# Kernel tuning notes

Hardware: AMD Instinct MI355X
Metric: run time of the kernel (lower is better)

Reference implementation:

```python
import jax, jax.numpy as jnp
import numpy as np

D_MODEL = 768; HEADS = 12; DEPTH = 12; PATCH = 16; IMG = 224; NCLS = 1000
N_PATCH = (IMG // PATCH) ** 2  # 196
N_TOK = N_PATCH + 1            # 197 (cls token)
REGION = 16                    # tokens per routing region
TOPK = 4                       # regions gathered per query region


def layernorm(x, g, b, eps=1e-5):
    mu = jnp.mean(x, -1, keepdims=True)
    var = jnp.mean((x - mu) ** 2, -1, keepdims=True)
    return (x - mu) * jax.lax.rsqrt(var + eps) * g + b


def biformer_attn(h, qkv_w, qkv_b, proj_w, proj_b):
    # Bi-Level Routing Attention: region-mean routing + top-k region gather.
    B, N, C = h.shape
    dh = C // HEADS
    qkv = h @ qkv_w + qkv_b                      # [B,N,3C]
    pad = (-N) % REGION
    qkv = jnp.pad(qkv, ((0, 0), (0, pad), (0, 0)))
    Np = N + pad; R = Np // REGION
    q, k, v = jnp.split(qkv, 3, axis=-1)
    qr = q.reshape(B, R, REGION, C)
    kr = k.reshape(B, R, REGION, C)
    vr = v.reshape(B, R, REGION, C)
    # coarse region-level affinity from region means
    q_reg = qr.mean(2); k_reg = kr.mean(2)       # [B,R,C]
    aff = jnp.einsum('brc,bsc->brs', q_reg, k_reg)
    _, idx = jax.lax.top_k(aff, TOPK)            # [B,R,TOPK] int32
    gather = jax.vmap(lambda t, i: t[i])         # gather regions per batch elem
    kg = gather(kr, idx).reshape(B, R, TOPK * REGION, C)
    vg = gather(vr, idx).reshape(B, R, TOPK * REGION, C)
    # fine-grained attention within each region over gathered keys
    qh = qr.reshape(B, R, REGION, HEADS, dh)
    kh = kg.reshape(B, R, TOPK * REGION, HEADS, dh)
    vh = vg.reshape(B, R, TOPK * REGION, HEADS, dh)
    att = jnp.einsum('brmhd,brnhd->bhrmn', qh, kh) * (dh ** -0.5)
    att = jax.nn.softmax(att, axis=-1)
    out = jnp.einsum('bhrmn,brnhd->brmhd', att, vh).reshape(B, Np, C)[:, :N]
    return out @ proj_w + proj_b


def _forward(x, conv_w, conv_b, cls_token, pos_embed,
             ln1_g, ln1_b, qkv_w, qkv_b, proj_w, proj_b,
             ln2_g, ln2_b, fc1_w, fc1_b, fc2_w, fc2_b, head_w, head_b):
    B = x.shape[0]
    p = jax.lax.conv_general_dilated(
        x, conv_w, (PATCH, PATCH), 'VALID',
        dimension_numbers=('NCHW', 'OIHW', 'NCHW')) + conv_b[None, :, None, None]
    t = p.reshape(B, D_MODEL, N_PATCH).transpose(0, 2, 1)   # [B,196,C]
    t = jnp.concatenate([jnp.broadcast_to(cls_token, (B, 1, D_MODEL)), t], axis=1)
    t = t + pos_embed                                        # [B,197,C]

    def block(xc, pp):
        g1, b1, qw, qb, pw, pb, g2, b2, f1w, f1b, f2w, f2b = pp
        h = layernorm(xc, g1, b1)
        h = biformer_attn(h, qw, qb, pw, pb)
        h = layernorm(h, g2, b2)
        h = jax.nn.gelu(h @ f1w + f1b, approximate=False) @ f2w + f2b
        return xc + h, None   # single residual around LN-Attn-LN-MLP (as in source)

    blk = (ln1_g, ln1_b, qkv_w, qkv_b, proj_w, proj_b,
           ln2_g, ln2_b, fc1_w, fc1_b, fc2_w, fc2_b)
    t, _ = jax.lax.scan(block, t, blk)
    return t[:, 0] @ head_w + head_b


def setup_inputs() -> dict:
    key = jax.random.key(0)
    ks = jax.random.split(key, 10)
    B = 16; s = 0.02
    f32 = jnp.float32
    return {
        'x': jax.random.normal(ks[0], (B, 3, IMG, IMG), f32),
        'conv_w': jax.random.normal(ks[1], (D_MODEL, 3, PATCH, PATCH), f32) * s,
        'conv_b': jnp.zeros((D_MODEL,), f32),
        'cls_token': jax.random.normal(ks[2], (1, 1, D_MODEL), f32) * s,
        'pos_embed': jax.random.normal(ks[3], (1, N_TOK, D_MODEL), f32) * s,
        'ln1_g': jnp.ones((DEPTH, D_MODEL), f32),
        'ln1_b': jnp.zeros((DEPTH, D_MODEL), f32),
        'qkv_w': jax.random.normal(ks[4], (DEPTH, D_MODEL, 3 * D_MODEL), f32) * s,
        'qkv_b': jnp.zeros((DEPTH, 3 * D_MODEL), f32),
        'proj_w': jax.random.normal(ks[5], (DEPTH, D_MODEL, D_MODEL), f32) * s,
        'proj_b': jnp.zeros((DEPTH, D_MODEL), f32),
        'ln2_g': jnp.ones((DEPTH, D_MODEL), f32),
        'ln2_b': jnp.zeros((DEPTH, D_MODEL), f32),
        'fc1_w': jax.random.normal(ks[6], (DEPTH, D_MODEL, 4 * D_MODEL), f32) * s,
        'fc1_b': jnp.zeros((DEPTH, 4 * D_MODEL), f32),
        'fc2_w': jax.random.normal(ks[7], (DEPTH, 4 * D_MODEL, D_MODEL), f32) * s,
        'fc2_b': jnp.zeros((DEPTH, D_MODEL), f32),
        'head_w': jax.random.normal(ks[8], (D_MODEL, NCLS), f32) * s,
        'head_b': jnp.zeros((NCLS,), f32),
    }


def reference(x, conv_w, conv_b, cls_token, pos_embed,
              ln1_g, ln1_b, qkv_w, qkv_b, proj_w, proj_b,
              ln2_g, ln2_b, fc1_w, fc1_b, fc2_w, fc2_b, head_w, head_b):
    return _forward(x, conv_w, conv_b, cls_token, pos_embed,
                    ln1_g, ln1_b, qkv_w, qkv_b, proj_w, proj_b,
                    ln2_g, ln2_b, fc1_w, fc1_b, fc2_w, fc2_b, head_w, head_b)
```

## Files before the change

### kernel.cpp

```cpp
#include <hip/hip_runtime.h>
#include <hip/hip_bf16.h>
#include <math.h>


typedef __bf16 bf16_t;
typedef __bf16 bf16x8 __attribute__((ext_vector_type(8)));
typedef __bf16 bf16x4 __attribute__((ext_vector_type(4)));
typedef __bf16 bf16x2v __attribute__((ext_vector_type(2)));
typedef float floatx4 __attribute__((ext_vector_type(4)));

static __device__ __forceinline__ float b2f(bf16_t x) { return (float)x; }
static __device__ __forceinline__ bf16_t f2b(float x) { return (bf16_t)x; }

#define AS1q __attribute__((address_space(1)))
#define AS3q __attribute__((address_space(3)))
static __device__ __forceinline__ void gll16(const bf16_t* g, bf16_t* l) {
    __builtin_amdgcn_global_load_lds((const AS1q void*)g, (AS3q void*)l, 16, 0, 0);
}

__global__ void transpose_split(const float* __restrict__ in, bf16_t* __restrict__ oh,
                                bf16_t* __restrict__ ol, int R, int C) {
    __shared__ float tile[32][33];
    int c0 = blockIdx.x * 32, r0 = blockIdx.y * 32;
    int tx = threadIdx.x, ty = threadIdx.y;
#pragma unroll
    for (int i = 0; i < 4; i++) {
        int r = r0 + ty + i * 8;
        float v = 0.f;
        if (r < R && (c0 + tx) < C) v = in[(size_t)r * C + c0 + tx];
        tile[ty + i * 8][tx] = v;
    }
    __syncthreads();
#pragma unroll
    for (int i = 0; i < 4; i++) {
        int c = c0 + ty + i * 8;
        if (c < C && (r0 + tx) < R) {
            float v = tile[tx][ty + i * 8];
            bf16_t h = f2b(v);
            oh[(size_t)c * R + r0 + tx] = h;
            ol[(size_t)c * R + r0 + tx] = f2b(v - b2f(h));
        }
    }
}

__global__ void split_kernel(const float* __restrict__ in, bf16_t* __restrict__ oh,
                             bf16_t* __restrict__ ol, int n) {
    int id = blockIdx.x * 256 + threadIdx.x;
    if (id < n) {
        float v = in[id];
        bf16_t h = f2b(v);
        oh[id] = h;
        ol[id] = f2b(v - b2f(h));
    }
}

__global__ void im2col_split(const float* __restrict__ x, bf16_t* __restrict__ oh,
                             bf16_t* __restrict__ ol) {
    int id = blockIdx.x * 256 + threadIdx.x;
    if (id >= 3136 * 768) return;
    int col = id % 768, row = id / 768;
    int b = row / 196, p = row % 196;
    int py = p / 14, px = p % 14;
    int c = col >> 8, rem = col & 255, ky = rem >> 4, kx = rem & 15;
    float v = x[(((size_t)(b * 3 + c)) * 224 + (py * 16 + ky)) * 224 + (px * 16 + kx)];
    bf16_t h = f2b(v);
    oh[id] = h;
    ol[id] = f2b(v - b2f(h));
}

__global__ void clspos_kernel(const float* __restrict__ cls, const float* __restrict__ pos,
                              float* __restrict__ t) {
    int id = blockIdx.x * 256 + threadIdx.x;
    int b = id / 768, c = id % 768;
    t[((size_t)(b * 197)) * 768 + c] = cls[c] + pos[c];
}

__global__ __launch_bounds__(256) void ln_kernel(const float* __restrict__ in,
                                                 const float* __restrict__ g,
                                                 const float* __restrict__ bb,
                                                 bf16_t* __restrict__ oh,
                                                 bf16_t* __restrict__ ol,
                                                 float* __restrict__ outf) {
    int row = blockIdx.x;
    int t = threadIdx.x;
    const float* x = in + (size_t)row * 768;
    float v0 = x[t], v1 = x[t + 256], v2 = x[t + 512];
    float s = v0 + v1 + v2;
#pragma unroll
    for (int off = 32; off > 0; off >>= 1) s += __shfl_down(s, off, 64);
    __shared__ float red[8];
    int lane = t & 63, wave = t >> 6;
    if (lane == 0) red[wave] = s;
    __syncthreads();
    float mu = (red[0] + red[1] + red[2] + red[3]) * (1.f / 768.f);
    float d0 = v0 - mu, d1 = v1 - mu, d2 = v2 - mu;
    float vs = d0 * d0 + d1 * d1 + d2 * d2;
#pragma unroll
    for (int off = 32; off > 0; off >>= 1) vs += __shfl_down(vs, off, 64);
    if (lane == 0) red[4 + wave] = vs;
    __syncthreads();
    float var = (red[4] + red[5] + red[6] + red[7]) * (1.f / 768.f);
    float rstd = 1.0f / sqrtf(var + 1e-5f);
    float y0 = d0 * rstd * g[t] + bb[t];
    float y1 = d1 * rstd * g[t + 256] + bb[t + 256];
    float y2 = d2 * rstd * g[t + 512] + bb[t + 512];
    size_t base = (size_t)row * 768;
    bf16_t h0 = f2b(y0), h1 = f2b(y1), h2 = f2b(y2);
    oh[base + t] = h0; oh[base + t + 256] = h1; oh[base + t + 512] = h2;
    ol[base + t] = f2b(y0 - b2f(h0));
    ol[base + t + 256] = f2b(y1 - b2f(h1));
    ol[base + t + 512] = f2b(y2 - b2f(h2));
    if (outf) {
        outf[base + t] = y0; outf[base + t + 256] = y1; outf[base + t + 512] = y2;
    }
}

__global__ __launch_bounds__(256) void gemm_nts(const bf16_t* __restrict__ Ah,
                                                const bf16_t* __restrict__ Al,
                                                const bf16_t* __restrict__ Bh,
                                                const bf16_t* __restrict__ Bl,
                                                const float* __restrict__ bias,
                                                float* __restrict__ outF,
                                                bf16_t* __restrict__ outHi,
                                                bf16_t* __restrict__ outLo,
                                                int M, int N, int K, int Kc,
                                                size_t pstride, int mode) {
    __shared__ __align__(16) bf16_t Ash[2][128 * 32];
    __shared__ __align__(16) bf16_t Asl[2][128 * 32];
    __shared__ __align__(16) bf16_t Bsh[2][128 * 32];
    __shared__ __align__(16) bf16_t Bsl[2][128 * 32];
    const int t = threadIdx.x;
    const int lane = t & 63, wave = t >> 6;
    const int quad = lane >> 4, l16 = lane & 15;
    const int wm = (wave >> 1) * 64, wn = (wave & 1) * 64;
    const int m0 = blockIdx.y * 128, n0 = blockIdx.x * 128;
    const int kz = blockIdx.z;

    floatx4 acc[4][4];
#pragma unroll
    for (int i = 0; i < 4; i++)
#pragma unroll
        for (int j = 0; j < 4; j++)
#pragma unroll
            for (int p = 0; p < 4; p++) acc[i][j][p] = 0.f;

    const int sr = wave * 16 + (lane >> 2);
    const int sc = (lane & 3) * 8;
    const size_t a0 = (size_t)(m0 + sr) * K + sc;
    const size_t a1 = (size_t)(m0 + 64 + sr) * K + sc;
    const size_t b0 = (size_t)(n0 + sr) * K + sc;
    const size_t b1 = (size_t)(n0 + 64 + sr) * K + sc;
    const int lo0 = wave * 512;
    const int lo1 = 2048 + wave * 512;

    auto stage = [&](int buf, int k) {
        gll16(Ah + a0 + k, &Ash[buf][lo0]);
        gll16(Ah + a1 + k, &Ash[buf][lo1]);
        gll16(Al + a0 + k, &Asl[buf][lo0]);
        gll16(Al + a1 + k, &Asl[buf][lo1]);
        gll16(Bh + b0 + k, &Bsh[buf][lo0]);
        gll16(Bh + b1 + k, &Bsh[buf][lo1]);
        gll16(Bl + b0 + k, &Bsl[buf][lo0]);
        gll16(Bl + b1 + k, &Bsl[buf][lo1]);
    };
    auto compute = [&](int buf) {
        bf16x8 ah[4], al[4], bh[4], bl[4];
#pragma unroll
        for (int i = 0; i < 4; i++) {
            ah[i] = *(const bf16x8*)&Ash[buf][(wm + i * 16 + l16) * 32 + quad * 8];
            al[i] = *(const bf16x8*)&Asl[buf][(wm + i * 16 + l16) * 32 + quad * 8];
        }
#pragma unroll
        for (int j = 0; j < 4; j++) {
            bh[j] = *(const bf16x8*)&Bsh[buf][(wn + j * 16 + l16) * 32 + quad * 8];
            bl[j] = *(const bf16x8*)&Bsl[buf][(wn + j * 16 + l16) * 32 + quad * 8];
        }
#pragma unroll
        for (int i = 0; i < 4; i++)
#pragma unroll
            for (int j = 0; j < 4; j++) {
                acc[i][j] = __builtin_amdgcn_mfma_f32_16x16x32_bf16(ah[i], bh[j], acc[i][j], 0, 0, 0);
                acc[i][j] = __builtin_amdgcn_mfma_f32_16x16x32_bf16(ah[i], bl[j], acc[i][j], 0, 0, 0);
                acc[i][j] = __builtin_amdgcn_mfma_f32_16x16x32_bf16(al[i], bh[j], acc[i][j], 0, 0, 0);
            }
    };

    const int kbeg = kz * Kc, kend = kbeg + Kc;
    stage(0, kbeg);
    __syncthreads();
    int cur = 0;
    for (int k0 = kbeg + 32; k0 < kend; k0 += 32) {
        stage(cur ^ 1, k0);
        compute(cur);
        __syncthreads();
        cur ^= 1;
    }
    compute(cur);

    float* Pp = outF + (size_t)kz * pstride;
#pragma unroll
    for (int i = 0; i < 4; i++) {
#pragma unroll
        for (int p = 0; p < 4; p++) {
            int m = m0 + wm + i * 16 + quad * 4 + p;
            if (m >= M) continue;
#pragma unroll
            for (int j = 0; j < 4; j++) {
                int n = n0 + wn + j * 16 + l16;
                if (n >= N) continue;
                if (mode == 0) {
                    Pp[(size_t)m * N + n] = acc[i][j][p];
                } else if (mode == 1) {
                    outF[(size_t)m * N + n] = acc[i][j][p] + bias[n];
                } else {
                    float v = acc[i][j][p] + bias[n];
                    float gl = 0.5f * v * (1.0f + erff(v * 0.70710678118654752f));
                    bf16_t h = f2b(gl);
                    outHi[(size_t)m * N + n] = h;
                    outLo[(size_t)m * N + n] = f2b(gl - b2f(h));
                }
            }
        }
    }
}

__global__ void reduce_kernel(const float* __restrict__ parts, int nchunks,
                              const float* __restrict__ bias, float* __restrict__ out,
                              const float* __restrict__ pos, int M, int N, int mode) {
    int id = blockIdx.x * 256 + threadIdx.x;
    int total = (M * N) >> 2;
    if (id >= total) return;
    size_t e = (size_t)id * 4;
    int n = (int)(e % N), m = (int)(e / N);
    size_t csz = (size_t)M * N;
    floatx4 s = *(const floatx4*)(parts + e);
    for (int c = 1; c < nchunks; c++) s += *(const floatx4*)(parts + (size_t)c * csz + e);
    s += *(const floatx4*)(bias + n);
    if (mode == 0) {
        *(floatx4*)(out + e) = s;
    } else if (mode == 1) {
        floatx4 o = *(const floatx4*)(out + e);
        *(floatx4*)(out + e) = o + s;
    } else {
        int b = m / 196, p = m % 196;
        floatx4 pv = *(const floatx4*)(pos + (size_t)(1 + p) * N + n);
        *(floatx4*)(out + ((size_t)(b * 197 + 1 + p)) * N + n) = s + pv;
    }
}

__global__ __launch_bounds__(256) void reduce_ln_kernel(const float* __restrict__ parts,
                                                        int nchunks, size_t cstride,
                                                        const float* __restrict__ bias,
                                                        const float* __restrict__ g,
                                                        const float* __restrict__ bb,
                                                        bf16_t* __restrict__ oh,
                                                        bf16_t* __restrict__ ol) {
    int row = blockIdx.x;
    int t = threadIdx.x;
    float y0, y1, y2;
    {
        size_t base = (size_t)row * 768;
        float a0 = bias[t], a1 = bias[t + 256], a2 = bias[t + 512];
        for (int c = 0; c < nchunks; c++) {
            const float* p = parts + (size_t)c * cstride + base;
            a0 += p[t]; a1 += p[t + 256]; a2 += p[t + 512];
        }
        y0 = a0; y1 = a1; y2 = a2;
    }
    float s = y0 + y1 + y2;
#pragma unroll
    for (int off = 32; off > 0; off >>= 1) s += __shfl_down(s, off, 64);
    __shared__ float red[8];
    int lane = t & 63, wave = t >> 6;
    if (lane == 0) red[wave] = s;
    __syncthreads();
    float mu = (red[0] + red[1] + red[2] + red[3]) * (1.f / 768.f);
    float d0 = y0 - mu, d1 = y1 - mu, d2 = y2 - mu;
    float vs = d0 * d0 + d1 * d1 + d2 * d2;
#pragma unroll
    for (int off = 32; off > 0; off >>= 1) vs += __shfl_down(vs, off, 64);
    if (lane == 0) red[4 + wave] = vs;
    __syncthreads();
    float var = (red[4] + red[5] + red[6] + red[7]) * (1.f / 768.f);
    float rstd = 1.0f / sqrtf(var + 1e-5f);
    float z0 = d0 * rstd * g[t] + bb[t];
    float z1 = d1 * rstd * g[t + 256] + bb[t + 256];
    float z2 = d2 * rstd * g[t + 512] + bb[t + 512];
    size_t base = (size_t)row * 768;
    bf16_t h0 = f2b(z0), h1 = f2b(z1), h2 = f2b(z2);
    oh[base + t] = h0; oh[base + t + 256] = h1; oh[base + t + 512] = h2;
    ol[base + t] = f2b(z0 - b2f(h0));
    ol[base + t + 256] = f2b(z1 - b2f(h1));
    ol[base + t + 512] = f2b(z2 - b2f(h2));
}

__global__ void regsum_kernel(const float* __restrict__ h, float* __restrict__ hsum) {
    int bid = blockIdx.x;
    int b = bid / 13, r = bid % 13;
    int t = threadIdx.x;
#pragma unroll
    for (int j = 0; j < 3; j++) {
        int c = t + j * 256;
        float s = 0.f;
        for (int tt = 0; tt < 16; tt++) {
            int tp = r * 16 + tt;
            if (tp < 197) s += h[((size_t)(b * 197 + tp)) * 768 + c];
        }
        hsum[(size_t)bid * 768 + c] = s;
    }
}

__global__ __launch_bounds__(256) void qkreg_gemm(const float* __restrict__ hsum,
                                                  const float* __restrict__ W,
                                                  const float* __restrict__ bias,
                                                  float* __restrict__ qreg,
                                                  float* __restrict__ kreg) {
    __shared__ float A_s[16][33];
    __shared__ float B_s[32][68];
    const int t = threadIdx.x;
    const int m0 = blockIdx.y * 16;
    const int n0 = blockIdx.x * 64;
    const int m = t >> 4;
    const int nn = (t & 15) * 4;
    floatx4 acc;
    acc[0] = acc[1] = acc[2] = acc[3] = 0.f;

    for (int k0 = 0; k0 < 768; k0 += 32) {
        {
            int c = (t & 15) * 2;
            A_s[t >> 4][c]     = hsum[(size_t)(m0 + (t >> 4)) * 768 + k0 + c];
            A_s[t >> 4][c + 1] = hsum[(size_t)(m0 + (t >> 4)) * 768 + k0 + c + 1];
        }
        {
            int kr = t >> 3, cc = (t & 7) * 8;
            const float* src = W + (size_t)(k0 + kr) * 2304 + n0 + cc;
            floatx4 w0 = *(const floatx4*)src;
            floatx4 w1 = *(const floatx4*)(src + 4);
            *(floatx4*)&B_s[kr][cc] = w0;
            *(floatx4*)&B_s[kr][cc + 4] = w1;
        }
        __syncthreads();
#pragma unroll
        for (int kk = 0; kk < 32; kk++) {
            float a = A_s[m][kk];
            floatx4 bv = *(const floatx4*)&B_s[kk][nn];
            acc += a * bv;
        }
        __syncthreads();
    }

    int row = m0 + m;
    int r = row % 13;
    float nr = (r == 12) ? 5.f : 16.f;
#pragma unroll
    for (int j = 0; j < 4; j++) {
        int c = n0 + nn + j;
        float val = (acc[j] + nr * bias[c]) * 0.0625f;
        if (c < 768) qreg[(size_t)row * 768 + c] = val;
        else         kreg[(size_t)row * 768 + (c - 768)] = val;
    }
}

__global__ __launch_bounds__(256) void afftopk_kernel(const float* __restrict__ qreg,
                                                      const float* __restrict__ kreg,
                                                      int* __restrict__ idx) {
    __shared__ float arow[16];
    int br = blockIdx.x;
    int b = br / 13;
    int t = threadIdx.x, lane = t & 63, w = t >> 6;
    const float* qp = qreg + (size_t)br * 768;
    for (int s = w; s < 13; s += 4) {
        const float* kp = kreg + ((size_t)(b * 13 + s)) * 768;
        float a = 0.f;
#pragma unroll
        for (int jj = 0; jj < 3; jj++) {
            floatx4 q4 = *(const floatx4*)&qp[lane * 4 + jj * 256];
            floatx4 k4 = *(const floatx4*)&kp[lane * 4 + jj * 256];
            a += q4[0] * k4[0] + q4[1] * k4[1] + q4[2] * k4[2] + q4[3] * k4[3];
        }
#pragma unroll
        for (int msk = 32; msk >= 1; msk >>= 1) a += __shfl_xor(a, msk, 64);
        if (lane == 0) arow[s] = a;
    }
    __syncthreads();
    if (t == 0) {
        int mask = 0;
#pragma unroll
        for (int k = 0; k < 4; k++) {
            float best = -3.4e38f;
            int bi = 0;
            for (int s = 0; s < 13; s++) {
                if (!((mask >> s) & 1) && arow[s] > best) { best = arow[s]; bi = s; }
            }
            mask |= 1 << bi;
            idx[br * 4 + k] = bi;
        }
    }
}

__global__ __launch_bounds__(256) void attn_kernel(const float* __restrict__ qkv,
                                                   const int* __restrict__ idx,
                                                   bf16_t* __restrict__ oh,
                                                   bf16_t* __restrict__ ol) {
    __shared__ __align__(16) bf16_t Qh[16 * 72], Ql[16 * 72];
    __shared__ __align__(16) bf16_t Kh[64 * 72], Kl[64 * 72];
    __shared__ __align__(16) bf16_t Vth[64 * 68], Vtl[64 * 68];
    __shared__ __align__(16) float P_s[16 * 68];

    int bid = blockIdx.x;
    int head = bid % 12;
    int r = (bid / 12) % 13;
    int b = bid / (12 * 13);
    int t = threadIdx.x;
    const int lane = t & 63, wave = t >> 6;
    const int quad = lane >> 4, l16 = lane & 15;
    const int co = head * 64;
    const size_t rowb = (size_t)(b * 197);

    int regs[4];
#pragma unroll
    for (int j = 0; j < 4; j++) regs[j] = idx[(b * 13 + r) * 4 + j];

    {
        int rh = t >> 5;
        int c2 = (t & 31) * 2;
#pragma unroll
        for (int it = 0; it < 2; it++) {
            int m = rh + it * 8;
            int tp = r * 16 + m;
            float2 v; v.x = 0.f; v.y = 0.f;
            if (tp < 197) v = *(const float2*)&qkv[(rowb + tp) * 2304 + co + c2];
            bf16_t h0 = f2b(v.x), h1 = f2b(v.y);
            bf16x2v hh = {h0, h1};
            bf16x2v ll = {f2b(v.x - b2f(h0)), f2b(v.y - b2f(h1))};
            *(bf16x2v*)&Qh[m * 72 + c2] = hh;
            *(bf16x2v*)&Ql[m * 72 + c2] = ll;
        }
#pragma unroll
        for (int nb = 0; nb < 4; nb++) {
            int reg = regs[nb];
#pragma unroll
            for (int i2 = 0; i2 < 2; i2++) {
                int nn = rh + i2 * 8;
                int tp = reg * 16 + nn;
                int n = nb * 16 + nn;
                float2 v; v.x = 0.f; v.y = 0.f;
                if (tp < 197) v = *(const float2*)&qkv[(rowb + tp) * 2304 + 768 + co + c2];
                bf16_t h0 = f2b(v.x), h1 = f2b(v.y);
                bf16x2v hh = {h0, h1};
                bf16x2v ll = {f2b(v.x - b2f(h0)), f2b(v.y - b2f(h1))};
                *(bf16x2v*)&Kh[n * 72 + c2] = hh;
                *(bf16x2v*)&Kl[n * 72 + c2] = ll;
            }
        }
    }
    {
        int d = lane;
#pragma unroll
        for (int nb = 0; nb < 4; nb++) {
            int reg = regs[nb];
#pragma unroll
            for (int i2 = 0; i2 < 4; i2++) {
                int nn = wave + i2 * 4;
                int tp = reg * 16 + nn;
                int n = nb * 16 + nn;
                float v = (tp < 197) ? qkv[(rowb + tp) * 2304 + 1536 + co + d] : 0.f;
                bf16_t h = f2b(v);
                Vth[d * 68 + n] = h;
                Vtl[d * 68 + n] = f2b(v - b2f(h));
            }
        }
    }
    __syncthreads();

    {
        const int j = wave;
        bf16x8 qfh[2], qfl[2], kfh[2], kfl[2];
#pragma unroll
        for (int ks = 0; ks < 2; ks++) {
            qfh[ks] = *(const bf16x8*)&Qh[l16 * 72 + ks * 32 + quad * 8];
            qfl[ks] = *(const bf16x8*)&Ql[l16 * 72 + ks * 32 + quad * 8];
            kfh[ks] = *(const bf16x8*)&Kh[(j * 16 + l16) * 72 + ks * 32 + quad * 8];
            kfl[ks] = *(const bf16x8*)&Kl[(j * 16 + l16) * 72 + ks * 32 + quad * 8];
        }
        floatx4 s;
        s[0] = s[1] = s[2] = s[3] = 0.f;
#pragma unroll
        for (int ks = 0; ks < 2; ks++) {
            s = __builtin_amdgcn_mfma_f32_16x16x32_bf16(qfh[ks], kfh[ks], s, 0, 0, 0);
            s = __builtin_amdgcn_mfma_f32_16x16x32_bf16(qfh[ks], kfl[ks], s, 0, 0, 0);
            s = __builtin_amdgcn_mfma_f32_16x16x32_bf16(qfl[ks], kfh[ks], s, 0, 0, 0);
        }
#pragma unroll
        for (int p = 0; p < 4; p++)
            P_s[(quad * 4 + p) * 68 + j * 16 + l16] = s[p] * 0.125f;
    }
    __syncthreads();

    {
        int rw = t >> 4, c = t & 15;
        floatx4 v = *(const floatx4*)&P_s[rw * 68 + c * 4];
        float mx = fmaxf(fmaxf(v[0], v[1]), fmaxf(v[2], v[3]));
#pragma unroll
        for (int msk = 8; msk >= 1; msk >>= 1) mx = fmaxf(mx, __shfl_xor(mx, msk, 64));
        floatx4 e;
        e[0] = expf(v[0] - mx); e[1] = expf(v[1] - mx);
        e[2] = expf(v[2] - mx); e[3] = expf(v[3] - mx);
        float sm = e[0] + e[1] + e[2] + e[3];
#pragma unroll
        for (int msk = 8; msk >= 1; msk >>= 1) sm += __shfl_xor(sm, msk, 64);
        float inv = 1.f / sm;
        e[0] *= inv; e[1] *= inv; e[2] *= inv; e[3] *= inv;
        *(floatx4*)&P_s[rw * 68 + c * 4] = e;
    }
    __syncthreads();

    {
        const int j = wave;
        bf16x8 pfh[2], pfl[2], vfh[2], vfl[2];
#pragma unroll
        for (int ks = 0; ks < 2; ks++) {
            floatx4 p0 = *(const floatx4*)&P_s[l16 * 68 + ks * 32 + quad * 8];
            floatx4 p1 = *(const floatx4*)&P_s[l16 * 68 + ks * 32 + quad * 8 + 4];
#pragma unroll
            for (int i = 0; i < 4; i++) {
                float f0 = p0[i], f1 = p1[i];
                bf16_t h0 = f2b(f0), h1 = f2b(f1);
                pfh[ks][i] = h0;      pfh[ks][4 + i] = h1;
                pfl[ks][i] = f2b(f0 - b2f(h0));
                pfl[ks][4 + i] = f2b(f1 - b2f(h1));
            }
            int vrow = (j * 16 + l16) * 68 + ks * 32 + quad * 8;
            bf16x4 a0 = *(const bf16x4*)&Vth[vrow];
            bf16x4 a1 = *(const bf16x4*)&Vth[vrow + 4];
            bf16x4 c0 = *(const bf16x4*)&Vtl[vrow];
            bf16x4 c1 = *(const bf16x4*)&Vtl[vrow + 4];
#pragma unroll
            for (int i = 0; i < 4; i++) {
                vfh[ks][i] = a0[i]; vfh[ks][4 + i] = a1[i];
                vfl[ks][i] = c0[i]; vfl[ks][4 + i] = c1[i];
            }
        }
        floatx4 o;
        o[0] = o[1] = o[2] = o[3] = 0.f;
#pragma unroll
        for (int ks = 0; ks < 2; ks++) {
            o = __builtin_amdgcn_mfma_f32_16x16x32_bf16(pfh[ks], vfh[ks], o, 0, 0, 0);
            o = __builtin_amdgcn_mfma_f32_16x16x32_bf16(pfh[ks], vfl[ks], o, 0, 0, 0);
            o = __builtin_amdgcn_mfma_f32_16x16x32_bf16(pfl[ks], vfh[ks], o, 0, 0, 0);
        }
#pragma unroll
        for (int p = 0; p < 4; p++) {
            int m = quad * 4 + p;
            int tp = r * 16 + m;
            if (tp < 197) {
                size_t oidx = (rowb + tp) * 768 + co + j * 16 + l16;
                float f = o[p];
                bf16_t h = f2b(f);
                oh[oidx] = h;
                ol[oidx] = f2b(f - b2f(h));
            }
        }
    }
}

__global__ void headx_split(const float* __restrict__ t, bf16_t* __restrict__ oh,
                            bf16_t* __restrict__ ol) {
    int id = blockIdx.x * 256 + threadIdx.x;
    if (id >= 16 * 768) return;
    int b = id / 768, c = id % 768;
    float v = t[((size_t)(b * 197)) * 768 + c];
    bf16_t h = f2b(v);
    oh[id] = h;
    ol[id] = f2b(v - b2f(h));
}

extern "C" void kernel_launch(void* const* d_in, const int* in_sizes, int n_in,
                              void* d_out, int out_size, void* d_ws, size_t ws_size,
                              hipStream_t stream) {
    const float* x      = (const float*)d_in[0];
    const float* conv_w = (const float*)d_in[1];
    const float* conv_b = (const float*)d_in[2];
    const float* cls    = (const float*)d_in[3];
    const float* pos    = (const float*)d_in[4];
    const float* ln1g   = (const float*)d_in[5];
    const float* ln1b   = (const float*)d_in[6];
    const float* qkvw   = (const float*)d_in[7];
    const float* qkvb   = (const float*)d_in[8];
    const float* projw  = (const float*)d_in[9];
    const float* projb  = (const float*)d_in[10];
    const float* ln2g   = (const float*)d_in[11];
    const float* ln2b   = (const float*)d_in[12];
    const float* fc1w   = (const float*)d_in[13];
    const float* fc1b   = (const float*)d_in[14];
    const float* fc2w   = (const float*)d_in[15];
    const float* fc2b   = (const float*)d_in[16];
    const float* headw  = (const float*)d_in[17];
    const float* headb  = (const float*)d_in[18];
    float* out = (float*)d_out;

    char* ws = (char*)d_ws;
    size_t off = 0;
    auto alloc = [&](size_t bytes) -> void* {
        void* p = ws + off;
        off += (bytes + 255) & ~(size_t)255;
        return p;
    };
    float*  tbuf   = (float*)alloc((size_t)3152 * 768 * 4);
    float*  h32    = (float*)alloc((size_t)3152 * 768 * 4);
    bf16_t* lnHi   = (bf16_t*)alloc((size_t)3152 * 768 * 2);
    bf16_t* lnLo   = (bf16_t*)alloc((size_t)3152 * 768 * 2);
    bf16_t* atHi   = (bf16_t*)alloc((size_t)3152 * 768 * 2);
    bf16_t* atLo   = (bf16_t*)alloc((size_t)3152 * 768 * 2);
    bf16_t* WhiT   = (bf16_t*)alloc((size_t)3072 * 768 * 2);
    bf16_t* WloT   = (bf16_t*)alloc((size_t)3072 * 768 * 2);
    char*   uni    = (char*)alloc((size_t)3152 * 3072 * 2 * 2);
    float*  qkvF   = (float*)uni;
    bf16_t* geHi   = (bf16_t*)uni;
    bf16_t* geLo   = geHi + (size_t)3152 * 3072;
    bf16_t* imHi   = (bf16_t*)uni;
    bf16_t* imLo   = imHi + (size_t)3136 * 768;
    float*  embPar = (float*)(uni + (size_t)3136 * 768 * 2 * 2);
    float*  hsum   = (float*)alloc((size_t)208 * 768 * 4);
    float*  qreg   = (float*)alloc((size_t)208 * 768 * 4);
    float*  kreg   = (float*)alloc((size_t)208 * 768 * 4);
    int*    idx    = (int*)alloc((size_t)832 * 4);
    bf16_t* hdHi   = (bf16_t*)alloc((size_t)16 * 768 * 2);
    bf16_t* hdLo   = (bf16_t*)alloc((size_t)16 * 768 * 2);
    alloc((size_t)1 << 18);
    if (off > ws_size) return;

    dim3 blk(256);
    dim3 tblk(32, 8);
    const int RED768 = (3152 * 768 / 4) / 256;
    const int REDEMB = (3136 * 768 / 4) / 256;
    const size_t PS = (size_t)3152 * 768;

    im2col_split<<<dim3(9408), blk, 0, stream>>>(x, imHi, imLo);
    split_kernel<<<dim3(2304), blk, 0, stream>>>(conv_w, WhiT, WloT, 768 * 768);
    gemm_nts<<<dim3(6, 25, 3), blk, 0, stream>>>(imHi, imLo, WhiT, WloT, nullptr,
                                                 embPar, nullptr, nullptr,
                                                 3136, 768, 768, 256, (size_t)3136 * 768, 0);
    reduce_kernel<<<dim3(REDEMB), blk, 0, stream>>>(embPar, 3, conv_b, tbuf, pos,
                                                    3136, 768, 2);
    clspos_kernel<<<dim3(48), blk, 0, stream>>>(cls, pos, tbuf);

    for (int l = 0; l < 12; l++) {
        ln_kernel<<<dim3(3152), blk, 0, stream>>>(tbuf, ln1g + l * 768, ln1b + l * 768,
                                                  lnHi, lnLo, h32);

        regsum_kernel<<<dim3(208), blk, 0, stream>>>(h32, hsum);
        qkreg_gemm<<<dim3(24, 13), blk, 0, stream>>>(hsum, qkvw + (size_t)l * 768 * 2304,
                                                     qkvb + l * 2304, qreg, kreg);
        afftopk_kernel<<<dim3(208), blk, 0, stream>>>(qreg, kreg, idx);

        transpose_split<<<dim3(72, 24), tblk, 0, stream>>>(qkvw + (size_t)l * 768 * 2304,
                                                           WhiT, WloT, 768, 2304);
        gemm_nts<<<dim3(18, 25, 1), blk, 0, stream>>>(lnHi, lnLo, WhiT, WloT,
                                                      qkvb + l * 2304, qkvF,
                                                      nullptr, nullptr,
                                                      3152, 2304, 768, 768, 0, 1);

        attn_kernel<<<dim3(16 * 13 * 12), blk, 0, stream>>>(qkvF, idx, atHi, atLo);

        transpose_split<<<dim3(24, 24), tblk, 0, stream>>>(projw + (size_t)l * 768 * 768,
                                                           WhiT, WloT, 768, 768);
        gemm_nts<<<dim3(6, 25, 4), blk, 0, stream>>>(atHi, atLo, WhiT, WloT, nullptr,
                                                     (float*)uni, nullptr, nullptr,
                                                     3152, 768, 768, 192, PS, 0);
        reduce_ln_kernel<<<dim3(3152), blk, 0, stream>>>((float*)uni, 4, PS,
                                                         projb + l * 768,
                                                         ln2g + l * 768, ln2b + l * 768,
                                                         lnHi, lnLo);

        transpose_split<<<dim3(96, 24), tblk, 0, stream>>>(fc1w + (size_t)l * 768 * 3072,
                                                           WhiT, WloT, 768, 3072);
        gemm_nts<<<dim3(24, 25, 1), blk, 0, stream>>>(lnHi, lnLo, WhiT, WloT,
                                                      fc1b + l * 3072, nullptr,
                                                      geHi, geLo, 3152, 3072, 768, 768, 0, 2);

        transpose_split<<<dim3(24, 96), tblk, 0, stream>>>(fc2w + (size_t)l * 3072 * 768,
                                                           WhiT, WloT, 3072, 768);
        gemm_nts<<<dim3(6, 25, 3), blk, 0, stream>>>(geHi, geLo, WhiT, WloT, nullptr,
                                                     h32, nullptr, nullptr,
                                                     3152, 768, 3072, 1024, PS, 0);
        reduce_kernel<<<dim3(RED768), blk, 0, stream>>>(h32, 3, fc2b + l * 768,
                                                        tbuf, nullptr, 3152, 768, 1);
    }

    headx_split<<<dim3(48), blk, 0, stream>>>(tbuf, hdHi, hdLo);
    transpose_split<<<dim3(32, 24), tblk, 0, stream>>>(headw, WhiT, WloT, 768, 1000);
    gemm_nts<<<dim3(8, 1, 3), blk, 0, stream>>>(hdHi, hdLo, WhiT, WloT, nullptr,
                                                hsum, nullptr, nullptr,
                                                16, 1000, 768, 256, (size_t)16 * 1000, 0);
    reduce_kernel<<<dim3(16), blk, 0, stream>>>(hsum, 3, headb, out, nullptr,
                                                16, 1000, 0);
}
```

Baseline: 5.240 ms.

## Batch per-layer weight transposes into one launch and single-buffer GEMM LDS

Replaces the four per-layer transpose_split launches with one transpose_all kernel that converts all of a layer's weights into a larger scratch buffer at distinct offsets, cutting launch count. Separately, the GEMM drops its double-buffered LDS prefetch in favour of a single buffer with syncs before and after each load. That halves LDS use and may allow higher occupancy, but global-load latency is no longer hidden behind MFMA work. The two ideas are unrelated and pull in different directions.

```diff
diff --git a/kernel.cpp b/kernel.cpp
--- a/kernel.cpp
+++ b/kernel.cpp
@@ -17,6 +17,11 @@
 static __device__ __forceinline__ void gll16(const bf16_t* g, bf16_t* l) {
     __builtin_amdgcn_global_load_lds((const AS1q void*)g, (AS3q void*)l, 16, 0, 0);
 }
+
+#define OPRJ 1769472
+#define OFC1 2359296
+#define OFC2 4718592
+#define WTSZ 7077888
 
 __global__ void transpose_split(const float* __restrict__ in, bf16_t* __restrict__ oh,
                                 bf16_t* __restrict__ ol, int R, int C) {
@@ -40,6 +45,34 @@
             oh[(size_t)c * R + r0 + tx] = h;
             ol[(size_t)c * R + r0 + tx] = f2b(v - b2f(h));
         }
+    }
+}
+
+__global__ void transpose_all(const float* __restrict__ qkvw,
+                              const float* __restrict__ projw,
+                              const float* __restrict__ fc1w,
+                              const float* __restrict__ fc2w,
+                              bf16_t* __restrict__ oh, bf16_t* __restrict__ ol) {
+    __shared__ float tile[32][33];
+    int id = blockIdx.x;
+    const float* in; int R, C, ctiles; size_t ooff;
+    if (id < 1728)      { in = qkvw;  R = 768;  C = 2304; ctiles = 72; ooff = 0; }
+    else if (id < 2304) { id -= 1728; in = projw; R = 768;  C = 768;  ctiles = 24; ooff = OPRJ; }
+    else if (id < 4608) { id -= 2304; in = fc1w;  R = 768;  C = 3072; ctiles = 96; ooff = OFC1; }
+    else                { id -= 4608; in = fc2w;  R = 3072; C = 768;  ctiles = 24; ooff = OFC2; }
+    int c0 = (id % ctiles) * 32, r0 = (id / ctiles) * 32;
+    int tx = threadIdx.x, ty = threadIdx.y;
+#pragma unroll
+    for (int i = 0; i < 4; i++)
+        tile[ty + i * 8][tx] = in[(size_t)(r0 + ty + i * 8) * C + c0 + tx];
+    __syncthreads();
+#pragma unroll
+    for (int i = 0; i < 4; i++) {
+        int c = c0 + ty + i * 8;
+        float v = tile[tx][ty + i * 8];
+        bf16_t h = f2b(v);
+        oh[ooff + (size_t)c * R + r0 + tx] = h;
+        ol[ooff + (size_t)c * R + r0 + tx] = f2b(v - b2f(h));
     }
 }
 
@@ -125,10 +158,10 @@
                                                 bf16_t* __restrict__ outLo,
                                                 int M, int N, int K, int Kc,
                                                 size_t pstride, int mode) {
-    __shared__ __align__(16) bf16_t Ash[2][128 * 32];
-    __shared__ __align__(16) bf16_t Asl[2][128 * 32];
-    __shared__ __align__(16) bf16_t Bsh[2][128 * 32];
-    __shared__ __align__(16) bf16_t Bsl[2][128 * 32];
+    __shared__ __align__(16) bf16_t Ash[128 * 32];
+    __shared__ __align__(16) bf16_t Asl[128 * 32];
+    __shared__ __align__(16) bf16_t Bsh[128 * 32];
+    __shared__ __align__(16) bf16_t Bsl[128 * 32];
     const int t = threadIdx.x;
     const int lane = t & 63, wave = t >> 6;
     const int quad = lane >> 4, l16 = lane & 15;
@@ -153,27 +186,28 @@
     const int lo0 = wave * 512;
     const int lo1 = 2048 + wave * 512;
 
-    auto stage = [&](int buf, int k) {
-        gll16(Ah + a0 + k, &Ash[buf][lo0]);
-        gll16(Ah + a1 + k, &Ash[buf][lo1]);
-        gll16(Al + a0 + k, &Asl[buf][lo0]);
-        gll16(Al + a1 + k, &Asl[buf][lo1]);
-        gll16(Bh + b0 + k, &Bsh[buf][lo0]);
-        gll16(Bh + b1 + k, &Bsh[buf][lo1]);
-        gll16(Bl + b0 + k, &Bsl[buf][lo0]);
-        gll16(Bl + b1 + k, &Bsl[buf][lo1]);
-    };
-    auto compute = [&](int buf) {
+    const int kend = kz * Kc + Kc;
+    for (int k0 = kz * Kc; k0 < kend; k0 += 32) {
+        __syncthreads();
+        gll16(Ah + a0 + k0, Ash + lo0);
+        gll16(Ah + a1 + k0, Ash + lo1);
+        gll16(Al + a0 + k0, Asl + lo0);
+        gll16(Al + a1 + k0, Asl + lo1);
+        gll16(Bh + b0 + k0, Bsh + lo0);
+        gll16(Bh + b1 + k0, Bsh + lo1);
+        gll16(Bl + b0 + k0, Bsl + lo0);
+        gll16(Bl + b1 + k0, Bsl + lo1);
+        __syncthreads();
         bf16x8 ah[4], al[4], bh[4], bl[4];
 #pragma unroll
         for (int i = 0; i < 4; i++) {
-            ah[i] = *(const bf16x8*)&Ash[buf][(wm + i * 16 + l16) * 32 + quad * 8];
-            al[i] = *(const bf16x8*)&Asl[buf][(wm + i * 16 + l16) * 32 + quad * 8];
+            ah[i] = *(const bf16x8*)&Ash[(wm + i * 16 + l16) * 32 + quad * 8];
+            al[i] = *(const bf16x8*)&Asl[(wm + i * 16 + l16) * 32 + quad * 8];
         }
 #pragma unroll
         for (int j = 0; j < 4; j++) {
-            bh[j] = *(const bf16x8*)&Bsh[buf][(wn + j * 16 + l16) * 32 + quad * 8];
-            bl[j] = *(const bf16x8*)&Bsl[buf][(wn + j * 16 + l16) * 32 + quad * 8];
+            bh[j] = *(const bf16x8*)&Bsh[(wn + j * 16 + l16) * 32 + quad * 8];
+            bl[j] = *(const bf16x8*)&Bsl[(wn + j * 16 + l16) * 32 + quad * 8];
         }
 #pragma unroll
         for (int i = 0; i < 4; i++)
@@ -183,19 +217,7 @@
                 acc[i][j] = __builtin_amdgcn_mfma_f32_16x16x32_bf16(ah[i], bl[j], acc[i][j], 0, 0, 0);
                 acc[i][j] = __builtin_amdgcn_mfma_f32_16x16x32_bf16(al[i], bh[j], acc[i][j], 0, 0, 0);
             }
-    };
-
-    const int kbeg = kz * Kc, kend = kbeg + Kc;
-    stage(0, kbeg);
-    __syncthreads();
-    int cur = 0;
-    for (int k0 = kbeg + 32; k0 < kend; k0 += 32) {
-        stage(cur ^ 1, k0);
-        compute(cur);
-        __syncthreads();
-        cur ^= 1;
-    }
-    compute(cur);
+    }
 
     float* Pp = outF + (size_t)kz * pstride;
 #pragma unroll
@@ -612,8 +634,8 @@
     bf16_t* lnLo   = (bf16_t*)alloc((size_t)3152 * 768 * 2);
     bf16_t* atHi   = (bf16_t*)alloc((size_t)3152 * 768 * 2);
     bf16_t* atLo   = (bf16_t*)alloc((size_t)3152 * 768 * 2);
-    bf16_t* WhiT   = (bf16_t*)alloc((size_t)3072 * 768 * 2);
-    bf16_t* WloT   = (bf16_t*)alloc((size_t)3072 * 768 * 2);
+    bf16_t* WhiT   = (bf16_t*)alloc((size_t)WTSZ * 2);
+    bf16_t* WloT   = (bf16_t*)alloc((size_t)WTSZ * 2);
     char*   uni    = (char*)alloc((size_t)3152 * 3072 * 2 * 2);
     float*  qkvF   = (float*)uni;
     bf16_t* geHi   = (bf16_t*)uni;
@@ -646,6 +668,12 @@
     clspos_kernel<<<dim3(48), blk, 0, stream>>>(cls, pos, tbuf);
 
     for (int l = 0; l < 12; l++) {
+        transpose_all<<<dim3(6912), tblk, 0, stream>>>(qkvw + (size_t)l * 768 * 2304,
+                                                       projw + (size_t)l * 768 * 768,
+                                                       fc1w + (size_t)l * 768 * 3072,
+                                                       fc2w + (size_t)l * 3072 * 768,
+                                                       WhiT, WloT);
+
         ln_kernel<<<dim3(3152), blk, 0, stream>>>(tbuf, ln1g + l * 768, ln1b + l * 768,
                                                   lnHi, lnLo, h32);
 
@@ -654,8 +682,6 @@
                                                      qkvb + l * 2304, qreg, kreg);
         afftopk_kernel<<<dim3(208), blk, 0, stream>>>(qreg, kreg, idx);
 
-        transpose_split<<<dim3(72, 24), tblk, 0, stream>>>(qkvw + (size_t)l * 768 * 2304,
-                                                           WhiT, WloT, 768, 2304);
         gemm_nts<<<dim3(18, 25, 1), blk, 0, stream>>>(lnHi, lnLo, WhiT, WloT,
                                                       qkvb + l * 2304, qkvF,
                                                       nullptr, nullptr,
@@ -663,26 +689,20 @@
 
         attn_kernel<<<dim3(16 * 13 * 12), blk, 0, stream>>>(qkvF, idx, atHi, atLo);
 
-        transpose_split<<<dim3(24, 24), tblk, 0, stream>>>(projw + (size_t)l * 768 * 768,
-                                                           WhiT, WloT, 768, 768);
-        gemm_nts<<<dim3(6, 25, 4), blk, 0, stream>>>(atHi, atLo, WhiT, WloT, nullptr,
-                                                     (float*)uni, nullptr, nullptr,
+        gemm_nts<<<dim3(6, 25, 4), blk, 0, stream>>>(atHi, atLo, WhiT + OPRJ, WloT + OPRJ,
+                                                     nullptr, (float*)uni, nullptr, nullptr,
                                                      3152, 768, 768, 192, PS, 0);
         reduce_ln_kernel<<<dim3(3152), blk, 0, stream>>>((float*)uni, 4, PS,
                                                          projb + l * 768,
                                                          ln2g + l * 768, ln2b + l * 768,
                                                          lnHi, lnLo);
 
-        transpose_split<<<dim3(96, 24), tblk, 0, stream>>>(fc1w + (size_t)l * 768 * 3072,
-                                                           WhiT, WloT, 768, 3072);
-        gemm_nts<<<dim3(24, 25, 1), blk, 0, stream>>>(lnHi, lnLo, WhiT, WloT,
+        gemm_nts<<<dim3(24, 25, 1), blk, 0, stream>>>(lnHi, lnLo, WhiT + OFC1, WloT + OFC1,
                                                       fc1b + l * 3072, nullptr,
                                                       geHi, geLo, 3152, 3072, 768, 768, 0, 2);
 
-        transpose_split<<<dim3(24, 96), tblk, 0, stream>>>(fc2w + (size_t)l * 3072 * 768,
-                                                           WhiT, WloT, 3072, 768);
-        gemm_nts<<<dim3(6, 25, 3), blk, 0, stream>>>(geHi, geLo, WhiT, WloT, nullptr,
-                                                     h32, nullptr, nullptr,
+        gemm_nts<<<dim3(6, 25, 3), blk, 0, stream>>>(geHi, geLo, WhiT + OFC2, WloT + OFC2,
+                                                     nullptr, h32, nullptr, nullptr,
                                                      3152, 768, 3072, 1024, PS, 0);
         reduce_kernel<<<dim3(RED768), blk, 0, stream>>>(h32, 3, fc2b + l * 768,
                                                         tbuf, nullptr, 3152, 768, 1);
```

New measurement: 4.444 ms. -15.2%, faster.
